# Kernel tuning notes

Hardware: AMD Instinct MI355X
Metric: run time of the kernel (lower is better)

Reference implementation:

```python
import jax, jax.numpy as jnp
import numpy as np

N = 10000          # nodes
E = 320000         # edges
C = 128            # num_features (channels per irrep)
RB = 8             # radial basis size
NS = 10            # num_species
HID = 64           # radial MLP hidden
NPATH = 5          # TP paths: 0x0->0, 0x1->1, 1x0->1, 1x1->0(dot), 1x1->1(cross)
EPS = 0.17677669529663687  # 1/sqrt(avg_degree=32)


def setup_inputs() -> dict:
    key = jax.random.key(0)
    ks = jax.random.split(key, 20)
    inp = {
        "vectors": jax.random.normal(ks[0], (E, 3), jnp.float32),
        "node_feats": jax.random.normal(ks[1], (N, C * 4), jnp.float32),
        "node_specie": jax.random.randint(ks[2], (N,), 0, NS),
        "radial_embedding": jax.random.normal(ks[3], (E, RB), jnp.float32),
        "senders": jax.random.randint(ks[4], (E,), 0, N),
        "receivers": jax.random.randint(ks[5], (E,), 0, N),
    }
    s = 1.0 / np.sqrt(C)
    inp["W_up_s"] = jax.random.normal(ks[6], (C, C), jnp.float32) * s
    inp["W_up_v"] = jax.random.normal(ks[7], (C, C), jnp.float32) * s
    inp["W_rad1"] = jax.random.normal(ks[8], (RB, HID), jnp.float32) / np.sqrt(RB)
    inp["W_rad2"] = jax.random.normal(ks[9], (HID, NPATH * C), jnp.float32) / np.sqrt(HID)
    inp["W_down_s"] = jax.random.normal(ks[10], (C, C), jnp.float32) * s
    inp["W_down_v"] = jax.random.normal(ks[11], (C, C), jnp.float32) * s
    inp["W_skip_s"] = jax.random.normal(ks[12], (NS, C, C), jnp.float32) * s
    inp["W_skip_v"] = jax.random.normal(ks[13], (NS, C, C), jnp.float32) * s
    inp["W_prod_s"] = jax.random.normal(ks[14], (NS, 3, C), jnp.float32)
    inp["W_prod_v"] = jax.random.normal(ks[15], (NS, 2, C), jnp.float32)
    inp["W_lin_s"] = jax.random.normal(ks[16], (C, C), jnp.float32) * s
    inp["W_lin_v"] = jax.random.normal(ks[17], (C, C), jnp.float32) * s
    inp["W_ro"] = jax.random.normal(ks[18], (C, 1), jnp.float32) * s
    return inp


def _mace_forward(vectors, node_feats, node_specie, radial_embedding, senders,
                  receivers, W_up_s, W_up_v, W_rad1, W_rad2, W_down_s, W_down_v,
                  W_skip_s, W_skip_v, W_prod_s, W_prod_v, W_lin_s, W_lin_v, W_ro):
    n = node_feats.shape[0]
    # split flat mul_ir layout: [C x 0e | C x 1o]
    s = node_feats[:, :C]                      # [N, C]
    v = node_feats[:, C:].reshape(n, C, 3)     # [N, C, 3]

    # --- skip connection (species-indexed linear, first=False) ---
    Ws = W_skip_s[node_specie]                 # [N, C, C]
    Wv = W_skip_v[node_specie]
    sc_s = jnp.einsum('nc,ncd->nd', s, Ws)
    sc_v = jnp.einsum('nci,ncd->ndi', v, Wv)

    # --- interaction: linear_up ---
    h_s = s @ W_up_s
    h_v = jnp.einsum('nci,cd->ndi', v, W_up_v)

    # spherical harmonics (component normalization): Y1 = sqrt(3)*r_hat
    norm = jnp.linalg.norm(vectors, axis=-1, keepdims=True)
    Y1 = jnp.sqrt(3.0) * vectors / (norm + 1e-9)           # [E, 3]

    # radial MLP -> per-edge, per-path, per-channel TP weights
    w = jax.nn.silu(radial_embedding @ W_rad1) @ W_rad2
    w = w.reshape(-1, NPATH, C)                            # [E, 5, C]

    # gather sender features, depthwise ('uvu') CG tensor product with Y
    s_j = h_s[senders]                                     # [E, C]
    v_j = h_v[senders]                                     # [E, C, 3]
    dot = jnp.einsum('eci,ei->ec', v_j, Y1)                # 1o x 1o -> 0e
    crs = jnp.cross(v_j, Y1[:, None, :])                   # 1o x 1o -> 1o
    m_s = w[:, 0] * s_j + w[:, 3] * dot                    # [E, C]
    m_v = (w[:, 1][:, :, None] * s_j[:, :, None] * Y1[:, None, :]
           + w[:, 2][:, :, None] * v_j
           + w[:, 4][:, :, None] * crs)                    # [E, C, 3]

    # scatter to receivers
    agg_s = jax.ops.segment_sum(m_s, receivers, num_segments=n)
    agg_v = jax.ops.segment_sum(m_v, receivers, num_segments=n)

    # linear_down + epsilon scaling
    f_s = (agg_s @ W_down_s) * EPS
    f_v = jnp.einsum('nci,cd->ndi', agg_v, W_down_v) * EPS

    # --- equivariant product basis (correlation=2, symmetric) ---
    # order-1 and order-2 symmetric contractions for (0e, 1o) inputs:
    # scalars: A_s, A_s^2, |A_v|^2 ; vectors: A_v, A_s * A_v
    B_s = jnp.stack([f_s, f_s * f_s, jnp.sum(f_v * f_v, axis=-1)], axis=1)  # [N,3,C]
    B_v = jnp.stack([f_v, f_s[:, :, None] * f_v], axis=1)                    # [N,2,C,3]
    p_s = jnp.einsum('nkc,nkc->nc', B_s, W_prod_s[node_specie])
    p_v = jnp.einsum('nkci,nkc->nci', B_v, W_prod_v[node_specie])
    out_s = p_s @ W_lin_s + sc_s
    out_v = jnp.einsum('nci,cd->ndi', p_v, W_lin_v) + sc_v

    # --- linear readout (not last layer): invariant 0e output ---
    node_outputs = out_s @ W_ro                            # [N, 1]
    new_feats = jnp.concatenate([out_s, out_v.reshape(n, C * 3)], axis=-1)
    return node_outputs, new_feats


def reference(vectors, node_feats, node_specie, radial_embedding, senders,
              receivers, W_up_s, W_up_v, W_rad1, W_rad2, W_down_s, W_down_v,
              W_skip_s, W_skip_v, W_prod_s, W_prod_v, W_lin_s, W_lin_v, W_ro):
    return _mace_forward(vectors, node_feats, node_specie, radial_embedding,
                         senders, receivers, W_up_s, W_up_v, W_rad1, W_rad2,
                         W_down_s, W_down_v, W_skip_s, W_skip_v, W_prod_s,
                         W_prod_v, W_lin_s, W_lin_v, W_ro)
```

## Files before the change

### kernel.cpp

```cpp
#include <hip/hip_runtime.h>
#include <hip/hip_bf16.h>


#define NN 10000
#define EE 320000
#define FEPS 0.17677669529663687f

typedef __attribute__((ext_vector_type(4))) float f32x4;
typedef __attribute__((ext_vector_type(8))) short s16x8;

__device__ __forceinline__ float bflo(unsigned u) { return __uint_as_float(u << 16); }
__device__ __forceinline__ float bfhi(unsigned u) { return __uint_as_float(u & 0xffff0000u); }
__device__ __forceinline__ unsigned short f2bu(float f) {
    unsigned u = __float_as_uint(f);
    return (unsigned short)((u + 0x7FFFu + ((u >> 16) & 1u)) >> 16);
}
__device__ __forceinline__ unsigned pack2(float a, float b) {
    return (unsigned)f2bu(a) | ((unsigned)f2bu(b) << 16);
}
__device__ __forceinline__ s16x8 pack8(float4 a, float4 b) {
    union { s16x8 v; unsigned short u[8]; } r;
    r.u[0] = f2bu(a.x); r.u[1] = f2bu(a.y); r.u[2] = f2bu(a.z); r.u[3] = f2bu(a.w);
    r.u[4] = f2bu(b.x); r.u[5] = f2bu(b.y); r.u[6] = f2bu(b.z); r.u[7] = f2bu(b.w);
    return r.v;
}

#define TWN (26 * 16384)
#define W2N (640 * 64)
#define PREPX 20
#define HISTB 1250
__global__ __launch_bounds__(256) void k_prep_hist(
    const float* __restrict__ Wus, const float* __restrict__ Wuv,
    const float* __restrict__ Wds, const float* __restrict__ Wdv,
    const float* __restrict__ Wls, const float* __restrict__ Wlv,
    const float* __restrict__ Wss, const float* __restrict__ Wsv,
    const float* __restrict__ W_rad2,
    unsigned short* __restrict__ T,
    unsigned short* __restrict__ w2t,
    const int* __restrict__ recv, int* __restrict__ cnt) {
    const int b = blockIdx.x, tid = threadIdx.x;
    if (b < 26) {
        __shared__ unsigned short tr[128][130];
        const int m = b;
        const float* src;
        if (m == 0) src = Wus; else if (m == 1) src = Wuv;
        else if (m == 2) src = Wds; else if (m == 3) src = Wdv;
        else if (m == 4) src = Wls; else if (m == 5) src = Wlv;
        else if (m < 16) src = Wss + (size_t)(m - 6) * 16384;
        else src = Wsv + (size_t)(m - 16) * 16384;
        for (int i = tid; i < 16384; i += 256) {
            const int c = i >> 7, d = i & 127;
            tr[d][c] = f2bu(src[i]);
        }
        __syncthreads();
        unsigned* o32 = (unsigned*)(T + (size_t)m * 16384);
        for (int i = tid; i < 8192; i += 256) {
            const int d = i >> 6, c2 = (i & 63) * 2;
            o32[i] = (unsigned)tr[d][c2] | ((unsigned)tr[d][c2 + 1] << 16);
        }
    } else if (b < 26 + PREPX) {
        for (int i = (b - 26) * 256 + tid; i < W2N; i += PREPX * 256) {
            const int n = i >> 6, k = i & 63;
            w2t[i] = f2bu(W_rad2[k * 640 + n]);
        }
    } else {
        const int e = (b - (26 + PREPX)) * 256 + tid;
        if (e < EE) {
            int r = recv[e];
            r = ((unsigned)r < NN) ? r : 0;
            atomicAdd(&cnt[r], 1);
        }
    }
}

__global__ __launch_bounds__(1024) void k_scan_spec(
    const int* __restrict__ cnt, int* __restrict__ offs, int* __restrict__ cur,
    const int* __restrict__ specie, int* __restrict__ perm,
    int2* __restrict__ tiles, int* __restrict__ ntiles) {
    __shared__ int sums[1024];
    __shared__ int hcnt[10], hbase[10], hcur[10], tbase[11];
    const int t = threadIdx.x;
    const int chunk = (NN + 1023) / 1024;
    const int start = t * chunk;
    int local = 0;
    for (int i = 0; i < chunk; i++) {
        int idx = start + i;
        if (idx < NN) local += cnt[idx];
    }
    sums[t] = local;
    __syncthreads();
    for (int ofs = 1; ofs < 1024; ofs <<= 1) {
        int u = (t >= ofs) ? sums[t - ofs] : 0;
        __syncthreads();
        sums[t] += u;
        __syncthreads();
    }
    int base = (t == 0) ? 0 : sums[t - 1];
    for (int i = 0; i < chunk; i++) {
        int idx = start + i;
        if (idx < NN) {
            offs[idx] = base;
            cur[idx] = base;
            base += cnt[idx];
        }
    }
    if (t == 0) offs[NN] = sums[1023];
    if (t < 10) hcnt[t] = 0;
    __syncthreads();
    for (int n = t; n < NN; n += 1024) {
        int s = specie[n];
        s = ((unsigned)s < 10) ? s : 0;
        atomicAdd(&hcnt[s], 1);
    }
    __syncthreads();
    if (t == 0) {
        int run = 0, tc = 0;
        for (int sp = 0; sp < 10; sp++) {
            hbase[sp] = run; hcur[sp] = run; run += hcnt[sp];
            tbase[sp] = tc;  tc += (hcnt[sp] + 15) >> 4;
        }
        tbase[10] = tc;
        *ntiles = tc;
    }
    __syncthreads();
    const int tc = tbase[10];
    for (int ti = t; ti < tc; ti += 1024) {
        int sp = 0;
        while (sp < 9 && ti >= tbase[sp + 1]) sp++;
        const int b = (ti - tbase[sp]) * 16;
        tiles[ti] = make_int2(hbase[sp] + b, (sp << 8) | min(16, hcnt[sp] - b));
    }
    for (int n = t; n < NN; n += 1024) {
        int s = specie[n];
        s = ((unsigned)s < 10) ? s : 0;
        int slot = atomicAdd(&hcur[s], 1);
        if ((unsigned)slot < NN) perm[slot] = n;
    }
}

__global__ __launch_bounds__(256) void k_fill_pre(
    const int* __restrict__ recv, int* __restrict__ cur, int* __restrict__ csr,
    const float* __restrict__ nf,
    const unsigned short* __restrict__ Tw,
    uint2* __restrict__ h4o) {
    if (blockIdx.x >= 625) {
        const int e = (blockIdx.x - 625) * 256 + threadIdx.x;
        if (e < EE) {
            int r = recv[e];
            r = ((unsigned)r < NN) ? r : 0;
            int slot = atomicAdd(&cur[r], 1);
            if ((unsigned)slot < EE) csr[slot] = e;
        }
        return;
    }
    const int tile = blockIdx.x;
    const int tid = threadIdx.x;
    const int lane = tid & 63, wv = tid >> 6;
    const int col = lane & 15, quad = lane >> 4;
    __shared__ float nfl[16][512];
    {
        const float4* src = (const float4*)(nf + (size_t)tile * 16 * 512);
        float4* dst = (float4*)nfl;
        for (int i = tid; i < 2048; i += 256) dst[i] = src[i];
    }
    __syncthreads();
    const float* rp = nfl[col];
    s16x8 Af[4][4];
#pragma unroll
    for (int kt = 0; kt < 4; kt++) {
        const int ko = kt * 32 + quad * 8;
        const float4 fa = *(const float4*)(rp + ko);
        const float4 fb = *(const float4*)(rp + ko + 4);
        Af[0][kt] = pack8(fa, fb);
#pragma unroll
        for (int i = 0; i < 3; i++) {
            union { s16x8 v; unsigned short u[8]; } A;
#pragma unroll
            for (int j = 0; j < 8; j++) A.u[j] = f2bu(rp[128 + 3 * (ko + j) + i]);
            Af[1 + i][kt] = A.v;
        }
    }
    const unsigned short* Ts = Tw;
    const unsigned short* Tv = Tw + 16384;
#pragma unroll
    for (int nt = 0; nt < 2; nt++) {
        const int d = 32 * wv + 16 * nt + col;
        f32x4 C[4];
#pragma unroll
        for (int m = 0; m < 4; m++) C[m] = (f32x4){0.f, 0.f, 0.f, 0.f};
#pragma unroll
        for (int kt = 0; kt < 4; kt++) {
            const int ko = kt * 32 + quad * 8;
            const s16x8 Bs = *(const s16x8*)&Ts[(size_t)d * 128 + ko];
            const s16x8 Bv = *(const s16x8*)&Tv[(size_t)d * 128 + ko];
            C[0] = __builtin_amdgcn_mfma_f32_16x16x32_bf16(Af[0][kt], Bs, C[0], 0, 0, 0);
#pragma unroll
            for (int i = 0; i < 3; i++)
                C[1 + i] = __builtin_amdgcn_mfma_f32_16x16x32_bf16(Af[1 + i][kt], Bv, C[1 + i], 0, 0, 0);
        }
        const int P = ((d >> 5) << 4) + (d & 15);
        const int half = (d >> 4) & 1;
#pragma unroll
        for (int reg = 0; reg < 4; reg++) {
            const int node = tile * 16 + quad * 4 + reg;
            h4o[((size_t)node * 64 + P) * 2 + half] =
                make_uint2(pack2(C[0][reg], C[1][reg]), pack2(C[2][reg], C[3][reg]));
        }
    }
}

#define EGRID 2560
__global__ __launch_bounds__(256, 2) void k_edge_mfma(
    const float* __restrict__ vectors,
    const float* __restrict__ radial,
    const int* __restrict__ senders,
    const float* __restrict__ W_rad1,
    const unsigned short* __restrict__ w2t,
    const uint4* __restrict__ h4q,
    const int* __restrict__ offs, const int* __restrict__ csr,
    unsigned short* __restrict__ aggb) {
    __shared__ unsigned short w1s[512];
    __shared__ float4 em[3][64];
    __shared__ float radl[3][64][8];
    __shared__ unsigned short hidb[2 * 64 * 72];
    const int tid = threadIdx.x;
    const int lane = tid & 63, wv = tid >> 6;
    const int row = lane & 15, quad = lane >> 4;
    const int sE = tid >> 2, st = tid & 3;
    for (int i = tid; i < 512; i += 256) w1s[i] = f2bu(W_rad1[i]);

    s16x8 Bf[2][5][2];
#pragma unroll
    for (int ti = 0; ti < 2; ti++) {
        const int t = 2 * wv + ti;
#pragma unroll
        for (int p = 0; p < 5; p++) {
            const unsigned short* bp =
                w2t + (size_t)(128 * p + 16 * t + row) * 64 + quad * 8;
            Bf[ti][p][0] = *(const s16x8*)(bp);
            Bf[ti][p][1] = *(const s16x8*)(bp + 32);
        }
    }

    int curN = blockIdx.x, curS = offs[curN], curD = offs[curN + 1] - curS, curC0 = 0;
    int nxtN = curN, nxtS = curS, nxtD = curD, nxtC0 = 0;
    {
        nxtC0 += 64;
        if (nxtC0 >= nxtD) {
            nxtN += EGRID;
            if (nxtN < NN) { nxtS = offs[nxtN]; nxtD = offs[nxtN + 1] - nxtS; }
            nxtC0 = 0;
        }
    }
    int nx2N = nxtN, nx2S = nxtS, nx2D = nxtD, nx2C0 = nxtC0;
    if (nx2N < NN) {
        nx2C0 += 64;
        if (nx2C0 >= nx2D) {
            nx2N += EGRID;
            if (nx2N < NN) { nx2S = offs[nx2N]; nx2D = offs[nx2N + 1] - nx2S; }
            nx2C0 = 0;
        }
    }

    if (st < 2) {
        const int gi = curC0 + sE;
        if (gi < curD) {
            int e = csr[curS + gi];
            e = ((unsigned)e < EE) ? e : 0;
            if (st == 0) {
                int j = senders[e];
                j = ((unsigned)j < NN) ? j : 0;
                const float vx = vectors[e * 3 + 0];
                const float vy = vectors[e * 3 + 1];
                const float vz = vectors[e * 3 + 2];
                const float inr = 1.7320508075688772f /
                    (sqrtf(vx * vx + vy * vy + vz * vz) + 1e-9f);
                em[0][sE] = make_float4(__int_as_float(j), vx * inr, vy * inr, vz * inr);
            } else {
                *(float4*)&radl[0][sE][0] = *(const float4*)(radial + (size_t)e * 8);
                *(float4*)&radl[0][sE][4] = *(const float4*)(radial + (size_t)e * 8 + 4);
            }
        } else {
            if (st == 0) em[0][sE] = make_float4(0.f, 0.f, 0.f, 0.f);
            else {
                *(float4*)&radl[0][sE][0] = make_float4(0.f, 0.f, 0.f, 0.f);
                *(float4*)&radl[0][sE][4] = make_float4(0.f, 0.f, 0.f, 0.f);
            }
        }
    }
    int eReg = -1;
    if (nxtN < NN && st < 2) {
        const int gi = nxtC0 + sE;
        if (gi < nxtD) {
            int e = csr[nxtS + gi];
            eReg = ((unsigned)e < EE) ? e : 0;
        }
    }
    __syncthreads();

    float acc_s[2] = {0.f, 0.f}, av0[2] = {0.f, 0.f},
          av1[2] = {0.f, 0.f}, av2[2] = {0.f, 0.f};
    int cs = 0, hbI = 0;
    while (true) {
        const int ws = (cs == 2) ? 0 : cs + 1;
        const bool hasNxt = (nxtN < NN);
        const float4* emc = em[cs];
        const float* emf = (const float*)emc;
        uint4 hqA[4];
#pragma unroll
        for (int rg = 0; rg < 4; rg++) {
            const int j = __float_as_int(emf[(quad * 4 + rg) * 4]);
            hqA[rg] = h4q[(size_t)j * 64 + (wv << 4) + row];
        }
        bool sv = false;
        float4 ra0 = make_float4(0.f, 0.f, 0.f, 0.f);
        float4 ra1 = make_float4(0.f, 0.f, 0.f, 0.f);
        if (hasNxt && st < 2 && eReg >= 0) {
            sv = true;
            const int e = eReg;
            if (st == 0) {
                int j = senders[e];
                j = ((unsigned)j < NN) ? j : 0;
                ra0 = make_float4(vectors[e * 3 + 0], vectors[e * 3 + 1],
                                  vectors[e * 3 + 2], __int_as_float(j));
            } else {
                ra0 = *(const float4*)(radial + (size_t)e * 8);
                ra1 = *(const float4*)(radial + (size_t)e * 8 + 4);
            }
        }
        int eRegN = -1;
        if (nx2N < NN && st < 2) {
            const int gi = nx2C0 + sE;
            if (gi < nx2D) {
                int e = csr[nx2S + gi];
                eRegN = ((unsigned)e < EE) ? e : 0;
            }
        }
        const int glimC = min(64, curD - curC0);
        {
            const int g16C = (glimC + 15) & ~15;
            unsigned short* hb = hidb + hbI * 4608;
            const int u0 = st * 16;
            if (sE < glimC) {
                float rr[8];
                *(float4*)&rr[0] = *(const float4*)&radl[cs][sE][0];
                *(float4*)&rr[4] = *(const float4*)&radl[cs][sE][4];
#pragma unroll
                for (int h = 0; h < 2; h++) {
                    float a[8];
#pragma unroll
                    for (int u = 0; u < 8; u++) a[u] = 0.f;
#pragma unroll
                    for (int r = 0; r < 8; r++) {
                        const uint4 wa = *(const uint4*)&w1s[r * 64 + u0 + h * 8];
                        const float f = rr[r];
                        a[0] += f * bflo(wa.x); a[1] += f * bfhi(wa.x);
                        a[2] += f * bflo(wa.y); a[3] += f * bfhi(wa.y);
                        a[4] += f * bflo(wa.z); a[5] += f * bfhi(wa.z);
                        a[6] += f * bflo(wa.w); a[7] += f * bfhi(wa.w);
                    }
                    unsigned o[4];
#pragma unroll
                    for (int k = 0; k < 4; k++) {
                        const float s0 = a[2 * k] / (1.f + __expf(-a[2 * k]));
                        const float s1 = a[2 * k + 1] / (1.f + __expf(-a[2 * k + 1]));
                        o[k] = pack2(s0, s1);
                    }
                    *(uint4*)&hb[sE * 72 + u0 + h * 8] = make_uint4(o[0], o[1], o[2], o[3]);
                }
            } else if (sE < g16C) {
                *(uint4*)&hb[sE * 72 + u0] = make_uint4(0, 0, 0, 0);
                *(uint4*)&hb[sE * 72 + u0 + 8] = make_uint4(0, 0, 0, 0);
            }
        }
        if (hasNxt && st < 2) {
            if (st == 0) {
                if (sv) {
                    const float vx = ra0.x, vy = ra0.y, vz = ra0.z;
                    const float inr = 1.7320508075688772f /
                        (sqrtf(vx * vx + vy * vy + vz * vz) + 1e-9f);
                    em[ws][sE] = make_float4(ra0.w, vx * inr, vy * inr, vz * inr);
                } else {
                    em[ws][sE] = make_float4(0.f, 0.f, 0.f, 0.f);
                }
            } else {
                *(float4*)&radl[ws][sE][0] = ra0;
                *(float4*)&radl[ws][sE][4] = ra1;
            }
        }
        __syncthreads();
        {
            __builtin_amdgcn_s_setprio(1);
            const unsigned short* hb = hidb + hbI * 4608;
            for (int g0 = 0; g0 < glimC; g0 += 16) {
                const s16x8 A0 = *(const s16x8*)&hb[(g0 + row) * 72 + quad * 8];
                const s16x8 A1 = *(const s16x8*)&hb[(g0 + row) * 72 + 32 + quad * 8];
                float4 mm[4];
#pragma unroll
                for (int rg = 0; rg < 4; rg++) mm[rg] = emc[g0 + quad * 4 + rg];
                const bool more = (g0 + 16) < glimC;
                uint4 hqB[4];
                if (more) {
#pragma unroll
                    for (int rg = 0; rg < 4; rg++) {
                        const int j = __float_as_int(emf[(g0 + 16 + quad * 4 + rg) * 4]);
                        hqB[rg] = h4q[(size_t)j * 64 + (wv << 4) + row];
                    }
                }
#pragma unroll
                for (int ti = 0; ti < 2; ti++) {
                    float sj[4], a0r[4], a1r[4], a2r[4];
#pragma unroll
                    for (int rg = 0; rg < 4; rg++) {
                        const unsigned wx = ti ? hqA[rg].z : hqA[rg].x;
                        const unsigned wy = ti ? hqA[rg].w : hqA[rg].y;
                        sj[rg] = bflo(wx); a0r[rg] = bfhi(wx);
                        a1r[rg] = bflo(wy); a2r[rg] = bfhi(wy);
                    }
#pragma unroll
                    for (int p = 0; p < 5; p++) {
                        f32x4 z = {0.f, 0.f, 0.f, 0.f};
                        z = __builtin_amdgcn_mfma_f32_16x16x32_bf16(A0, Bf[ti][p][0], z, 0, 0, 0);
                        z = __builtin_amdgcn_mfma_f32_16x16x32_bf16(A1, Bf[ti][p][1], z, 0, 0, 0);
#pragma unroll
                        for (int rg = 0; rg < 4; rg++) {
                            const float w = z[rg];
                            const float y0 = mm[rg].y, y1 = mm[rg].z, y2 = mm[rg].w;
                            if (p == 0) {
                                acc_s[ti] += w * sj[rg];
                            } else if (p == 1) {
                                const float wsj = w * sj[rg];
                                av0[ti] += wsj * y0;
                                av1[ti] += wsj * y1;
                                av2[ti] += wsj * y2;
                            } else if (p == 2) {
                                av0[ti] += w * a0r[rg];
                                av1[ti] += w * a1r[rg];
                                av2[ti] += w * a2r[rg];
                            } else if (p == 3) {
                                acc_s[ti] += w * (a0r[rg] * y0 + a1r[rg] * y1 +
                                                  a2r[rg] * y2);
                            } else {
                                av0[ti] += w * (a1r[rg] * y2 - a2r[rg] * y1);
                                av1[ti] += w * (a2r[rg] * y0 - a0r[rg] * y2);
                                av2[ti] += w * (a0r[rg] * y1 - a1r[rg] * y0);
                            }
                        }
                    }
                }
                if (more) {
#pragma unroll
                    for (int rg = 0; rg < 4; rg++) hqA[rg] = hqB[rg];
                }
            }
            __builtin_amdgcn_s_setprio(0);
            if (curC0 + 64 >= curD) {
#pragma unroll
                for (int ti = 0; ti < 2; ti++) {
                    acc_s[ti] += __shfl_xor(acc_s[ti], 16); acc_s[ti] += __shfl_xor(acc_s[ti], 32);
                    av0[ti] += __shfl_xor(av0[ti], 16);     av0[ti] += __shfl_xor(av0[ti], 32);
                    av1[ti] += __shfl_xor(av1[ti], 16);     av1[ti] += __shfl_xor(av1[ti], 32);
                    av2[ti] += __shfl_xor(av2[ti], 16);     av2[ti] += __shfl_xor(av2[ti], 32);
                }
                if (lane < 16) {
                    unsigned short* og = aggb + (size_t)curN * 512;
#pragma unroll
                    for (int ti = 0; ti < 2; ti++) {
                        const int cc = 16 * (2 * wv + ti) + lane;
                        og[cc] = f2bu(acc_s[ti]);
                        og[128 + cc] = f2bu(av0[ti]);
                        og[256 + cc] = f2bu(av1[ti]);
                        og[384 + cc] = f2bu(av2[ti]);
                    }
                }
                acc_s[0] = acc_s[1] = 0.f; av0[0] = av0[1] = 0.f;
                av1[0] = av1[1] = 0.f;     av2[0] = av2[1] = 0.f;
            }
        }
        if (!hasNxt) break;
        curN = nxtN; curS = nxtS; curD = nxtD; curC0 = nxtC0;
        nxtN = nx2N; nxtS = nx2S; nxtD = nx2D; nxtC0 = nx2C0;
        if (nx2N < NN) {
            nx2C0 += 64;
            if (nx2C0 >= nx2D) {
                nx2N += EGRID;
                if (nx2N < NN) { nx2S = offs[nx2N]; nx2D = offs[nx2N + 1] - nx2S; }
                nx2C0 = 0;
            }
        }
        eReg = eRegN;
        cs = ws; hbI ^= 1;
    }
}

__global__ __launch_bounds__(256) void k_post_mfma(
    const float* __restrict__ nf,
    const unsigned short* __restrict__ aggb,
    const int* __restrict__ perm,
    const int2* __restrict__ tiles,
    const int* __restrict__ ntiles,
    const unsigned short* __restrict__ Tw,
    const float* __restrict__ Wps,
    const float* __restrict__ Wpv,
    const float* __restrict__ Wro,
    float* __restrict__ dout) {
    const int tile = blockIdx.x;
    if (tile >= *ntiles) return;
    const int2 td = tiles[tile];
    const int base = td.x, sp = td.y >> 8, cnt = td.y & 255;
    __shared__ int nodesl[16];
    __shared__ float rol[16];
    __shared__ unsigned short Pl[4][16][128];
    __shared__ float nfl[16][512];
    const int tid = threadIdx.x;
    if (tid < 16) {
        nodesl[tid] = perm[base + ((tid < cnt) ? tid : 0)];
        rol[tid] = 0.f;
    }
    __syncthreads();
    {
        float4* dst = (float4*)nfl;
        for (int i = tid; i < 2048; i += 256) {
            const int r = i >> 7, off = i & 127;
            dst[i] = ((const float4*)(nf + (size_t)nodesl[r] * 512))[off];
        }
    }
    __syncthreads();
    const int lane = tid & 63, wv = tid >> 6;
    const int col = lane & 15, quad = lane >> 4;
    const int aN = nodesl[col];
    const unsigned short* Tds = Tw + (size_t)2 * 16384;
    const unsigned short* Tdv = Tw + (size_t)3 * 16384;
    const unsigned short* Tls = Tw + (size_t)4 * 16384;
    const unsigned short* Tlv = Tw + (size_t)5 * 16384;
    const unsigned short* Tss = Tw + (size_t)(6 + sp) * 16384;
    const unsigned short* Tsv = Tw + (size_t)(16 + sp) * 16384;
    const float* rp = nfl[col];
    f32x4 SC[2][4];
#pragma unroll
    for (int nt = 0; nt < 2; nt++) {
        const int d = 32 * wv + 16 * nt + col;
        f32x4 CF[4];
#pragma unroll
        for (int m = 0; m < 4; m++) CF[m] = (f32x4){0.f, 0.f, 0.f, 0.f};
#pragma unroll
        for (int kt = 0; kt < 4; kt++) {
            const int ko = kt * 32 + quad * 8;
            const s16x8 Bs = *(const s16x8*)&Tds[(size_t)d * 128 + ko];
            const s16x8 Bv = *(const s16x8*)&Tdv[(size_t)d * 128 + ko];
#pragma unroll
            for (int m = 0; m < 4; m++) {
                const s16x8 A = *(const s16x8*)&aggb[(size_t)aN * 512 + m * 128 + ko];
                CF[m] = __builtin_amdgcn_mfma_f32_16x16x32_bf16(A, m ? Bv : Bs, CF[m], 0, 0, 0);
            }
        }
        const float wps0 = Wps[sp * 384 + d];
        const float wps1 = Wps[sp * 384 + 128 + d];
        const float wps2 = Wps[sp * 384 + 256 + d];
        const float wpv0 = Wpv[sp * 256 + d];
        const float wpv1 = Wpv[sp * 256 + 128 + d];
#pragma unroll
        for (int reg = 0; reg < 4; reg++) {
            const float fs = CF[0][reg] * FEPS;
            const float f0 = CF[1][reg] * FEPS;
            const float f1 = CF[2][reg] * FEPS;
            const float f2 = CF[3][reg] * FEPS;
            const float ps = fs * wps0 + fs * fs * wps1 + (f0 * f0 + f1 * f1 + f2 * f2) * wps2;
            const float pb = wpv0 + fs * wpv1;
            const int r = quad * 4 + reg;
            Pl[0][r][d] = f2bu(ps);
            Pl[1][r][d] = f2bu(f0 * pb);
            Pl[2][r][d] = f2bu(f1 * pb);
            Pl[3][r][d] = f2bu(f2 * pb);
        }
        f32x4 CS[4];
#pragma unroll
        for (int m = 0; m < 4; m++) CS[m] = (f32x4){0.f, 0.f, 0.f, 0.f};
#pragma unroll
        for (int kt = 0; kt < 4; kt++) {
            const int ko = kt * 32 + quad * 8;
            const s16x8 Bss = *(const s16x8*)&Tss[(size_t)d * 128 + ko];
            const s16x8 Bsv = *(const s16x8*)&Tsv[(size_t)d * 128 + ko];
            const float4 fa = *(const float4*)(rp + ko);
            const float4 fb = *(const float4*)(rp + ko + 4);
            CS[0] = __builtin_amdgcn_mfma_f32_16x16x32_bf16(pack8(fa, fb), Bss, CS[0], 0, 0, 0);
#pragma unroll
            for (int i = 0; i < 3; i++) {
                union { s16x8 v; unsigned short u[8]; } A;
#pragma unroll
                for (int j = 0; j < 8; j++) A.u[j] = f2bu(rp[128 + 3 * (ko + j) + i]);
                CS[1 + i] = __builtin_amdgcn_mfma_f32_16x16x32_bf16(A.v, Bsv, CS[1 + i], 0, 0, 0);
            }
        }
#pragma unroll
        for (int m = 0; m < 4; m++) SC[nt][m] = CS[m];
    }
    __syncthreads();
#pragma unroll
    for (int nt = 0; nt < 2; nt++) {
        const int d = 32 * wv + 16 * nt + col;
        f32x4 CL[4];
#pragma unroll
        for (int m = 0; m < 4; m++) CL[m] = (f32x4){0.f, 0.f, 0.f, 0.f};
#pragma unroll
        for (int kt = 0; kt < 4; kt++) {
            const int ko = kt * 32 + quad * 8;
            const s16x8 Bls = *(const s16x8*)&Tls[(size_t)d * 128 + ko];
            const s16x8 Blv = *(const s16x8*)&Tlv[(size_t)d * 128 + ko];
#pragma unroll
            for (int m = 0; m < 4; m++) {
                const s16x8 A = *(const s16x8*)&Pl[m][col][ko];
                CL[m] = __builtin_amdgcn_mfma_f32_16x16x32_bf16(A, m ? Blv : Bls, CL[m], 0, 0, 0);
            }
        }
        const float wro = Wro[d];
#pragma unroll
        for (int reg = 0; reg < 4; reg++) {
            const int r = quad * 4 + reg;
            if (r < cnt) {
                const int node = nodesl[r];
                const float outs = CL[0][reg] + SC[nt][0][reg];
                const float o0 = CL[1][reg] + SC[nt][1][reg];
                const float o1 = CL[2][reg] + SC[nt][2][reg];
                const float o2 = CL[3][reg] + SC[nt][3][reg];
                float* o = dout + NN + (size_t)node * 512;
                o[d] = outs;
                o[128 + 3 * d + 0] = o0;
                o[128 + 3 * d + 1] = o1;
                o[128 + 3 * d + 2] = o2;
                atomicAdd(&rol[r], outs * wro);
            }
        }
    }
    __syncthreads();
    if (tid < 16 && tid < cnt) dout[nodesl[tid]] = rol[tid];
}

extern "C" void kernel_launch(void* const* d_in, const int* in_sizes, int n_in,
                              void* d_out, int out_size, void* d_ws, size_t ws_size,
                              hipStream_t stream) {
    const float* vectors    = (const float*)d_in[0];
    const float* node_feats = (const float*)d_in[1];
    const int*   specie     = (const int*)d_in[2];
    const float* radial     = (const float*)d_in[3];
    const int*   senders    = (const int*)d_in[4];
    const int*   receivers  = (const int*)d_in[5];
    const float* W_up_s     = (const float*)d_in[6];
    const float* W_up_v     = (const float*)d_in[7];
    const float* W_rad1     = (const float*)d_in[8];
    const float* W_rad2     = (const float*)d_in[9];
    const float* W_down_s   = (const float*)d_in[10];
    const float* W_down_v   = (const float*)d_in[11];
    const float* W_skip_s   = (const float*)d_in[12];
    const float* W_skip_v   = (const float*)d_in[13];
    const float* W_prod_s   = (const float*)d_in[14];
    const float* W_prod_v   = (const float*)d_in[15];
    const float* W_lin_s    = (const float*)d_in[16];
    const float* W_lin_v    = (const float*)d_in[17];
    const float* W_ro       = (const float*)d_in[18];
    float* out = (float*)d_out;

    char* w = (char*)d_ws;
    auto align256 = [](size_t x) { return (x + 255) & ~(size_t)255; };
    int* cnt  = (int*)w;              w += align256((size_t)NN * 4);
    int* offs = (int*)w;              w += align256((size_t)(NN + 1) * 4);
    int* cur  = (int*)w;              w += align256((size_t)NN * 4);
    int* csr  = (int*)w;              w += align256((size_t)EE * 4);
    uint4* h4q = (uint4*)w;           w += align256((size_t)NN * 64 * 16);
    unsigned short* aggb = (unsigned short*)w;  w += align256((size_t)NN * 512 * 2);
    unsigned short* w2t  = (unsigned short*)w;  w += align256((size_t)W2N * 2);
    unsigned short* Tw   = (unsigned short*)w;  w += align256((size_t)TWN * 2);
    int* perm   = (int*)w;            w += align256((size_t)NN * 4);
    int2* tiles = (int2*)w;           w += align256((size_t)640 * 8);
    int* ntiles = (int*)w;            w += align256(4);

    hipMemsetAsync(cnt, 0, (size_t)NN * 4, stream);
    k_prep_hist<<<26 + PREPX + HISTB, 256, 0, stream>>>(
        W_up_s, W_up_v, W_down_s, W_down_v, W_lin_s, W_lin_v,
        W_skip_s, W_skip_v, W_rad2, Tw, w2t, receivers, cnt);
    k_scan_spec<<<1, 1024, 0, stream>>>(cnt, offs, cur, specie, perm, tiles, ntiles);
    k_fill_pre<<<625 + HISTB, 256, 0, stream>>>(receivers, cur, csr,
                                                node_feats, Tw, (uint2*)h4q);
    k_edge_mfma<<<EGRID, 256, 0, stream>>>(vectors, radial, senders, W_rad1,
                                           w2t, h4q, offs, csr, aggb);
    k_post_mfma<<<640, 256, 0, stream>>>(node_feats, aggb, perm, tiles, ntiles,
                                         Tw, W_prod_s, W_prod_v, W_ro, out);
}
```

Measured before the change: 393.2 us.

## Move species skip-connection GEMM into pre-edge kernel, store to workspace

The species-dependent skip-connection matmul now runs in the pre-edge kernel. That kernel is re-tiled by species-sorted node tiles, so the bf16-packed node feature fragments it already builds for the up-projection are reused. The fp32 result is written to a new workspace buffer, and the post kernel reads it back instead of reloading node features and recomputing. This removes a second gather of node features and the repeated bf16 packing in the post kernel. In exchange it adds about 20 MB of fp32 write plus read traffic and a gathered node access pattern in the pre kernel.

```diff
diff --git a/kernel.cpp b/kernel.cpp
--- a/kernel.cpp
+++ b/kernel.cpp
@@ -142,9 +142,12 @@
     const int* __restrict__ recv, int* __restrict__ cur, int* __restrict__ csr,
     const float* __restrict__ nf,
     const unsigned short* __restrict__ Tw,
-    uint2* __restrict__ h4o) {
-    if (blockIdx.x >= 625) {
-        const int e = (blockIdx.x - 625) * 256 + threadIdx.x;
+    uint2* __restrict__ h4o,
+    const int* __restrict__ perm, const int2* __restrict__ tiles,
+    const int* __restrict__ ntiles,
+    float4* __restrict__ sc4) {
+    if (blockIdx.x >= 640) {
+        const int e = (blockIdx.x - 640) * 256 + threadIdx.x;
         if (e < EE) {
             int r = recv[e];
             r = ((unsigned)r < NN) ? r : 0;
@@ -154,16 +157,24 @@
         return;
     }
     const int tile = blockIdx.x;
+    if (tile >= *ntiles) return;
+    const int2 td = tiles[tile];
+    const int base = td.x, sp = td.y >> 8, cnt16 = td.y & 255;
+    __shared__ int nodesl[16];
+    __shared__ float nfl[16][512];
     const int tid = threadIdx.x;
+    if (tid < 16) nodesl[tid] = perm[base + ((tid < cnt16) ? tid : 0)];
+    __syncthreads();
+    {
+        float4* dst = (float4*)nfl;
+        for (int i = tid; i < 2048; i += 256) {
+            const int r = i >> 7, off = i & 127;
+            dst[i] = ((const float4*)(nf + (size_t)nodesl[r] * 512))[off];
+        }
+    }
+    __syncthreads();
     const int lane = tid & 63, wv = tid >> 6;
     const int col = lane & 15, quad = lane >> 4;
-    __shared__ float nfl[16][512];
-    {
-        const float4* src = (const float4*)(nf + (size_t)tile * 16 * 512);
-        float4* dst = (float4*)nfl;
-        for (int i = tid; i < 2048; i += 256) dst[i] = src[i];
-    }
-    __syncthreads();
     const float* rp = nfl[col];
     s16x8 Af[4][4];
 #pragma unroll
@@ -182,6 +193,8 @@
     }
     const unsigned short* Ts = Tw;
     const unsigned short* Tv = Tw + 16384;
+    const unsigned short* Tss = Tw + (size_t)(6 + sp) * 16384;
+    const unsigned short* Tsv = Tw + (size_t)(16 + sp) * 16384;
 #pragma unroll
     for (int nt = 0; nt < 2; nt++) {
         const int d = 32 * wv + 16 * nt + col;
@@ -202,9 +215,28 @@
         const int half = (d >> 4) & 1;
 #pragma unroll
         for (int reg = 0; reg < 4; reg++) {
-            const int node = tile * 16 + quad * 4 + reg;
+            const int node = nodesl[quad * 4 + reg];
             h4o[((size_t)node * 64 + P) * 2 + half] =
                 make_uint2(pack2(C[0][reg], C[1][reg]), pack2(C[2][reg], C[3][reg]));
+        }
+        f32x4 CS[4];
+#pragma unroll
+        for (int m = 0; m < 4; m++) CS[m] = (f32x4){0.f, 0.f, 0.f, 0.f};
+#pragma unroll
+        for (int kt = 0; kt < 4; kt++) {
+            const int ko = kt * 32 + quad * 8;
+            const s16x8 Bss = *(const s16x8*)&Tss[(size_t)d * 128 + ko];
+            const s16x8 Bsv = *(const s16x8*)&Tsv[(size_t)d * 128 + ko];
+            CS[0] = __builtin_amdgcn_mfma_f32_16x16x32_bf16(Af[0][kt], Bss, CS[0], 0, 0, 0);
+#pragma unroll
+            for (int i = 0; i < 3; i++)
+                CS[1 + i] = __builtin_amdgcn_mfma_f32_16x16x32_bf16(Af[1 + i][kt], Bsv, CS[1 + i], 0, 0, 0);
+        }
+#pragma unroll
+        for (int reg = 0; reg < 4; reg++) {
+            const int node = nodesl[quad * 4 + reg];
+            sc4[(size_t)node * 128 + d] =
+                make_float4(CS[0][reg], CS[1][reg], CS[2][reg], CS[3][reg]);
         }
     }
 }
@@ -494,7 +526,6 @@
 }
 
 __global__ __launch_bounds__(256) void k_post_mfma(
-    const float* __restrict__ nf,
     const unsigned short* __restrict__ aggb,
     const int* __restrict__ perm,
     const int2* __restrict__ tiles,
@@ -503,6 +534,7 @@
     const float* __restrict__ Wps,
     const float* __restrict__ Wpv,
     const float* __restrict__ Wro,
+    const float4* __restrict__ sc4,
     float* __restrict__ dout) {
     const int tile = blockIdx.x;
     if (tile >= *ntiles) return;
@@ -511,19 +543,10 @@
     __shared__ int nodesl[16];
     __shared__ float rol[16];
     __shared__ unsigned short Pl[4][16][128];
-    __shared__ float nfl[16][512];
     const int tid = threadIdx.x;
     if (tid < 16) {
         nodesl[tid] = perm[base + ((tid < cnt) ? tid : 0)];
         rol[tid] = 0.f;
-    }
-    __syncthreads();
-    {
-        float4* dst = (float4*)nfl;
-        for (int i = tid; i < 2048; i += 256) {
-            const int r = i >> 7, off = i & 127;
-            dst[i] = ((const float4*)(nf + (size_t)nodesl[r] * 512))[off];
-        }
     }
     __syncthreads();
     const int lane = tid & 63, wv = tid >> 6;
@@ -533,10 +556,6 @@
     const unsigned short* Tdv = Tw + (size_t)3 * 16384;
     const unsigned short* Tls = Tw + (size_t)4 * 16384;
     const unsigned short* Tlv = Tw + (size_t)5 * 16384;
-    const unsigned short* Tss = Tw + (size_t)(6 + sp) * 16384;
-    const unsigned short* Tsv = Tw + (size_t)(16 + sp) * 16384;
-    const float* rp = nfl[col];
-    f32x4 SC[2][4];
 #pragma unroll
     for (int nt = 0; nt < 2; nt++) {
         const int d = 32 * wv + 16 * nt + col;
@@ -573,27 +592,6 @@
             Pl[2][r][d] = f2bu(f1 * pb);
             Pl[3][r][d] = f2bu(f2 * pb);
         }
-        f32x4 CS[4];
-#pragma unroll
-        for (int m = 0; m < 4; m++) CS[m] = (f32x4){0.f, 0.f, 0.f, 0.f};
-#pragma unroll
-        for (int kt = 0; kt < 4; kt++) {
-            const int ko = kt * 32 + quad * 8;
-            const s16x8 Bss = *(const s16x8*)&Tss[(size_t)d * 128 + ko];
-            const s16x8 Bsv = *(const s16x8*)&Tsv[(size_t)d * 128 + ko];
-            const float4 fa = *(const float4*)(rp + ko);
-            const float4 fb = *(const float4*)(rp + ko + 4);
-            CS[0] = __builtin_amdgcn_mfma_f32_16x16x32_bf16(pack8(fa, fb), Bss, CS[0], 0, 0, 0);
-#pragma unroll
-            for (int i = 0; i < 3; i++) {
-                union { s16x8 v; unsigned short u[8]; } A;
-#pragma unroll
-                for (int j = 0; j < 8; j++) A.u[j] = f2bu(rp[128 + 3 * (ko + j) + i]);
-                CS[1 + i] = __builtin_amdgcn_mfma_f32_16x16x32_bf16(A.v, Bsv, CS[1 + i], 0, 0, 0);
-            }
-        }
-#pragma unroll
-        for (int m = 0; m < 4; m++) SC[nt][m] = CS[m];
     }
     __syncthreads();
 #pragma unroll
@@ -619,10 +617,11 @@
             const int r = quad * 4 + reg;
             if (r < cnt) {
                 const int node = nodesl[r];
-                const float outs = CL[0][reg] + SC[nt][0][reg];
-                const float o0 = CL[1][reg] + SC[nt][1][reg];
-                const float o1 = CL[2][reg] + SC[nt][2][reg];
-                const float o2 = CL[3][reg] + SC[nt][3][reg];
+                const float4 scv = sc4[(size_t)node * 128 + d];
+                const float outs = CL[0][reg] + scv.x;
+                const float o0 = CL[1][reg] + scv.y;
+                const float o1 = CL[2][reg] + scv.z;
+                const float o2 = CL[3][reg] + scv.w;
                 float* o = dout + NN + (size_t)node * 512;
                 o[d] = outs;
                 o[128 + 3 * d + 0] = o0;
@@ -673,16 +672,18 @@
     int* perm   = (int*)w;            w += align256((size_t)NN * 4);
     int2* tiles = (int2*)w;           w += align256((size_t)640 * 8);
     int* ntiles = (int*)w;            w += align256(4);
+    float4* sc4 = (float4*)w;         w += align256((size_t)NN * 128 * 16);
 
     hipMemsetAsync(cnt, 0, (size_t)NN * 4, stream);
     k_prep_hist<<<26 + PREPX + HISTB, 256, 0, stream>>>(
         W_up_s, W_up_v, W_down_s, W_down_v, W_lin_s, W_lin_v,
         W_skip_s, W_skip_v, W_rad2, Tw, w2t, receivers, cnt);
     k_scan_spec<<<1, 1024, 0, stream>>>(cnt, offs, cur, specie, perm, tiles, ntiles);
-    k_fill_pre<<<625 + HISTB, 256, 0, stream>>>(receivers, cur, csr,
-                                                node_feats, Tw, (uint2*)h4q);
+    k_fill_pre<<<640 + HISTB, 256, 0, stream>>>(
+        receivers, cur, csr, node_feats, Tw, (uint2*)h4q,
+        perm, tiles, ntiles, sc4);
     k_edge_mfma<<<EGRID, 256, 0, stream>>>(vectors, radial, senders, W_rad1,
                                            w2t, h4q, offs, csr, aggb);
-    k_post_mfma<<<640, 256, 0, stream>>>(node_feats, aggb, perm, tiles, ntiles,
-                                         Tw, W_prod_s, W_prod_v, W_ro, out);
-}
+    k_post_mfma<<<640, 256, 0, stream>>>(aggb, perm, tiles, ntiles,
+                                         Tw, W_prod_s, W_prod_v, W_ro, sc4, out);
+}
```

New measurement: 356.5 us. -9.3%, faster.
